# Performance work log

Hardware: AMD Instinct MI355X
Metric: run time of the kernel (lower is better)

The kernel has to match this reference:

```python
import jax, jax.numpy as jnp
import numpy as np

N_HEAD = 12

def setup_inputs() -> dict:
    key = jax.random.key(0)
    k1, k2, k3 = jax.random.split(key, 3)
    B, T, C = 8, 1024, 768
    x = jax.random.normal(k1, (B, T, C), dtype=jnp.float32)
    # torch nn.Linear weight layout: [out_features, in_features]
    W_attn = jax.random.normal(k2, (3 * C, C), dtype=jnp.float32) * 0.02
    b_attn = jax.random.normal(k3, (3 * C,), dtype=jnp.float32) * 0.02
    return {"x": x, "W_attn": W_attn, "b_attn": b_attn}

def reference(x, W_attn, b_attn):
    B, T, C = x.shape
    H = N_HEAD
    hs = C // H
    scale = 1.0 / jnp.sqrt(jnp.asarray(hs, x.dtype))
    # fused qkv projection: x @ W^T + b  -> [B, T, 3C]
    qkv = jnp.einsum('btc,oc->bto', x, W_attn) + b_attn
    qkv = qkv.reshape(B, T, 3, H, hs).transpose(2, 0, 3, 1, 4)  # [3, B, H, T, hs]
    q, k, v = qkv[0], qkv[1], qkv[2]
    scores = jnp.einsum('bhqd,bhkd->bhqk', q, k) * scale  # [B, H, T, T]
    causal = jnp.tril(jnp.ones((T, T), dtype=bool))
    # masked_fill(-inf) followed by ReLU == zero out masked positions after ReLU
    att = jnp.where(causal, jax.nn.relu(scores), jnp.zeros((), scores.dtype))
    y = jnp.einsum('bhqk,bhkd->bhqd', att, v)  # [B, H, T, hs]
    return y.transpose(0, 2, 1, 3).reshape(B, T, C)
```

## Files before the change

kernel.cpp:

```cpp
#include <hip/hip_runtime.h>
#include <hip/hip_bf16.h>
#include <stdint.h>

#define T_ 1024
#define C_ 768
#define H_ 12
#define HS 64

typedef __attribute__((ext_vector_type(8))) short bf16x8;
typedef __attribute__((ext_vector_type(4))) float f32x4;

#define GLOAD16(g, l) __builtin_amdgcn_global_load_lds( \
    (const __attribute__((address_space(1))) uint32_t*)(g), \
    (__attribute__((address_space(3))) uint32_t*)(l), 16, 0, 0)

#define WAITCNT_VM(n) asm volatile("s_waitcnt vmcnt(" #n ")" ::: "memory")

__device__ __forceinline__ ushort f2b(float f) {
  uint32_t u = __builtin_bit_cast(uint32_t, f);
  u = (u + 0x7fffu + ((u >> 16) & 1u)) >> 16;
  return (ushort)u;
}

__global__ __launch_bounds__(256) void cvt_bf16(
    const float* __restrict__ x, const float* __restrict__ wt,
    ushort* __restrict__ xb, ushort* __restrict__ wb) {
  const int NX4 = 8192 * 768 / 4;
  const int NW4 = 2304 * 768 / 4;
  int i = blockIdx.x * 256 + threadIdx.x;
  int stride = gridDim.x * 256;
  for (int idx = i; idx < NX4; idx += stride) {
    float4 f = ((const float4*)x)[idx];
    ushort4 o;
    o.x = f2b(f.x); o.y = f2b(f.y); o.z = f2b(f.z); o.w = f2b(f.w);
    ((ushort4*)xb)[idx] = o;
  }
  for (int idx = i; idx < NW4; idx += stride) {
    float4 f = ((const float4*)wt)[idx];
    ushort4 o;
    o.x = f2b(f.x); o.y = f2b(f.y); o.z = f2b(f.z); o.w = f2b(f.w);
    ((ushort4*)wb)[idx] = o;
  }
}

__global__ __launch_bounds__(256) void qkv_gemm(
    const ushort* __restrict__ xb, const ushort* __restrict__ wb,
    const float* __restrict__ bias,
    ushort* __restrict__ qo, ushort* __restrict__ ko, ushort* __restrict__ vT) {
  __shared__ __align__(16) char smem[49152];
  const int tid = threadIdx.x, lane = tid & 63, w = tid >> 6;
  const int g = lane >> 4, l15 = lane & 15;
  const int id = blockIdx.x;
  const int wg = (id & 7) * 144 + (id >> 3);
  const int m0 = (wg / 18) * 128, n0 = (wg % 18) * 128;
  const int wr = w >> 1, wc = w & 1;
  f32x4 acc[4][4] = {};

  const ushort* srcA[2];
  const ushort* srcB[2];
  int dstoff[2];
  #pragma unroll
  for (int c = 0; c < 2; ++c) {
    int p = (c * 4 + w) * 64 + lane;
    int row = p >> 2, s = p & 3;
    int sc = (s ^ ((row >> 1) & 3)) * 8;
    srcA[c] = xb + (size_t)(m0 + row) * 768 + sc;
    srcB[c] = wb + (size_t)(n0 + row) * 768 + sc;
    dstoff[c] = (c * 4 + w) * 1024;
  }

#define STAGE_G(bb_, k0) do { \
    _Pragma("unroll") \
    for (int c_ = 0; c_ < 2; ++c_) { \
      GLOAD16(srcA[c_] + (k0), (bb_) + dstoff[c_]); \
      GLOAD16(srcB[c_] + (k0), (bb_) + 8192 + dstoff[c_]); \
    } \
  } while (0)

#define GEMM_COMPUTE(cb_) do { \
    bf16x8 af[4], bfr[4]; \
    _Pragma("unroll") \
    for (int mi = 0; mi < 4; ++mi) { \
      int r_ = wr * 64 + mi * 16 + l15; \
      af[mi] = *(const bf16x8*)((cb_) + r_ * 64 + ((g ^ ((r_ >> 1) & 3)) << 4)); \
    } \
    _Pragma("unroll") \
    for (int ni = 0; ni < 4; ++ni) { \
      int r_ = wc * 64 + ni * 16 + l15; \
      bfr[ni] = *(const bf16x8*)((cb_) + 8192 + r_ * 64 + ((g ^ ((r_ >> 1) & 3)) << 4)); \
    } \
    __builtin_amdgcn_s_setprio(1); \
    _Pragma("unroll") \
    for (int mi = 0; mi < 4; ++mi) \
      _Pragma("unroll") \
      for (int ni = 0; ni < 4; ++ni) \
        acc[mi][ni] = __builtin_amdgcn_mfma_f32_16x16x32_bf16(af[mi], bfr[ni], acc[mi][ni], 0, 0, 0); \
    __builtin_amdgcn_s_setprio(0); \
  } while (0)

  STAGE_G(smem, 0);
  STAGE_G(smem + 16384, 32);
  char* cptr = smem;
  char* sptr = smem + 32768;
  for (int kk = 0; kk < 23; ++kk) {
    WAITCNT_VM(4);
    __builtin_amdgcn_s_barrier();
    if (kk < 22) STAGE_G(sptr, (kk + 2) * 32);
    GEMM_COMPUTE(cptr);
    cptr += 16384; if (cptr == smem + 49152) cptr = smem;
    sptr += 16384; if (sptr == smem + 49152) sptr = smem;
  }
  WAITCNT_VM(0);
  __builtin_amdgcn_s_barrier();
  GEMM_COMPUTE(cptr);
  __syncthreads();

  const int which = n0 / 768;
  if (which < 2) {
    ushort* outp = (which == 0) ? qo : ko;
    #pragma unroll
    for (int ni = 0; ni < 4; ++ni) {
      float bn = bias[n0 + wc * 64 + ni * 16 + l15];
      int nl = wc * 64 + ni * 16 + l15;
      #pragma unroll
      for (int mi = 0; mi < 4; ++mi) {
        #pragma unroll
        for (int r = 0; r < 4; ++r) {
          int ml = wr * 64 + mi * 16 + g * 4 + r;
          *(ushort*)(smem + ml * 256 + ((nl * 2) ^ ((ml & 7) << 4))) =
              f2b(acc[mi][ni][r] + bn);
        }
      }
    }
    __syncthreads();
    #pragma unroll
    for (int c = 0; c < 8; ++c) {
      int p = c * 256 + tid;
      int ml = p >> 4, nch = p & 15;
      uint4 val = *(const uint4*)(smem + ml * 256 + ((nch * 16) ^ ((ml & 7) << 4)));
      int m = m0 + ml;
      int nin = n0 + nch * 8 - which * 768;
      int h = nin >> 6, d = nin & 63;
      *(uint4*)(outp + ((size_t)((m >> 10) * H_ + h) * T_ + (m & (T_ - 1))) * HS + d) = val;
    }
  } else {
    #pragma unroll
    for (int ni = 0; ni < 4; ++ni) {
      float bn = bias[n0 + wc * 64 + ni * 16 + l15];
      int dl = wc * 64 + ni * 16 + l15;
      #pragma unroll
      for (int mi = 0; mi < 4; ++mi) {
        #pragma unroll
        for (int r = 0; r < 4; ++r) {
          int tl = wr * 64 + mi * 16 + g * 4 + r;
          *(ushort*)(smem + dl * 256 + ((tl * 2) ^ ((dl & 7) << 4))) =
              f2b(acc[mi][ni][r] + bn);
        }
      }
    }
    __syncthreads();
    const int b = m0 >> 10, t0base = m0 & 1023;
    #pragma unroll
    for (int c = 0; c < 8; ++c) {
      int p = c * 256 + tid;
      int dl = p >> 4, tch = p & 15;
      uint4 val = *(const uint4*)(smem + dl * 256 + ((tch * 16) ^ ((dl & 7) << 4)));
      int nin = n0 + dl - 1536;
      int h = nin >> 6, dd = nin & 63;
      *(uint4*)(vT + (((size_t)(b * H_ + h) * HS + dd) << 10) + t0base + tch * 8) = val;
    }
  }
}

__global__ __launch_bounds__(256) void attn_relu(
    const ushort* __restrict__ q, const ushort* __restrict__ k,
    const ushort* __restrict__ vT, float* __restrict__ out) {
  __shared__ __align__(16) char smem[57344];
  const int tid = threadIdx.x, lane = tid & 63, w = tid >> 6;
  const int g = lane >> 4, l15 = lane & 15;
  const int id = blockIdx.x;
  const int wg = (id & 7) * 192 + (id >> 3);
  const int bh = wg >> 4;
  const int qt = 15 - (wg & 15);
  const int q0 = qt * 64;
  const size_t base = (size_t)bh * (T_ * HS);
  const int qrow = w * 16 + l15;

  bf16x8 qf[2];
  #pragma unroll
  for (int kd = 0; kd < 2; ++kd)
    qf[kd] = *(const bf16x8*)(q + base + (size_t)(q0 + qrow) * HS + (kd * 4 + g) * 8);

  int rowS[2], scS[2], dstoff[2];
  #pragma unroll
  for (int c = 0; c < 2; ++c) {
    int p = (c * 4 + w) * 64 + lane;
    rowS[c] = p >> 3;
    scS[c] = ((p & 7) ^ (rowS[c] & 7)) * 8;
    dstoff[c] = (c * 4 + w) * 1024;
  }

#define STAGE_KV(bb_, kt) do { \
    _Pragma("unroll") \
    for (int c_ = 0; c_ < 2; ++c_) { \
      GLOAD16(k + base + (size_t)((kt) * 64 + rowS[c_]) * HS + scS[c_], (bb_) + dstoff[c_]); \
      GLOAD16(vT + base + (size_t)rowS[c_] * T_ + (kt) * 64 + scS[c_], (bb_) + 8192 + dstoff[c_]); \
    } \
  } while (0)

  f32x4 yacc[4] = {};
  char* const Pb = smem + 49152;

#define ATTN_COMPUTE(cb_, kt) do { \
    const char* Kb = (cb_); \
    const char* Vb = (cb_) + 8192; \
    f32x4 sacc[4] = {}; \
    __builtin_amdgcn_s_setprio(1); \
    _Pragma("unroll") \
    for (int kd = 0; kd < 2; ++kd) { \
      _Pragma("unroll") \
      for (int nt = 0; nt < 4; ++nt) { \
        int kr = nt * 16 + l15; \
        bf16x8 kf = *(const bf16x8*)(Kb + kr * 128 + (((kd * 4 + g) ^ (kr & 7)) << 4)); \
        sacc[nt] = __builtin_amdgcn_mfma_f32_16x16x32_bf16(qf[kd], kf, sacc[nt], 0, 0, 0); \
      } \
    } \
    __builtin_amdgcn_s_setprio(0); \
    _Pragma("unroll") \
    for (int nt = 0; nt < 4; ++nt) { \
      int kj = (kt) * 64 + nt * 16 + l15; \
      _Pragma("unroll") \
      for (int r = 0; r < 4; ++r) { \
        int i_ = w * 16 + g * 4 + r; \
        float sv = sacc[nt][r] * 0.125f; \
        float pv = (kj <= q0 + i_) ? fmaxf(sv, 0.0f) : 0.0f; \
        *(ushort*)(Pb + i_ * 128 + (((nt * 16 + l15) * 2) ^ ((i_ & 7) << 4))) = f2b(pv); \
      } \
    } \
    bf16x8 pf[2], vf[2][4]; \
    _Pragma("unroll") \
    for (int kj2 = 0; kj2 < 2; ++kj2) { \
      pf[kj2] = *(const bf16x8*)(Pb + qrow * 128 + (((kj2 * 4 + g) ^ (qrow & 7)) << 4)); \
      _Pragma("unroll") \
      for (int nt = 0; nt < 4; ++nt) { \
        int vr = nt * 16 + l15; \
        vf[kj2][nt] = *(const bf16x8*)(Vb + vr * 128 + (((kj2 * 4 + g) ^ (vr & 7)) << 4)); \
      } \
    } \
    __builtin_amdgcn_s_setprio(1); \
    _Pragma("unroll") \
    for (int kj2 = 0; kj2 < 2; ++kj2) \
      _Pragma("unroll") \
      for (int nt = 0; nt < 4; ++nt) \
        yacc[nt] = __builtin_amdgcn_mfma_f32_16x16x32_bf16(pf[kj2], vf[kj2][nt], yacc[nt], 0, 0, 0); \
    __builtin_amdgcn_s_setprio(0); \
  } while (0)

  const int nkt = qt + 1;
  STAGE_KV(smem, 0);
  if (nkt > 1) STAGE_KV(smem + 16384, 1);
  char* cptr = smem;
  char* sptr = smem + 32768;
  for (int kt = 0; kt < nkt - 1; ++kt) {
    WAITCNT_VM(4);
    __builtin_amdgcn_s_barrier();
    if (kt + 2 < nkt) STAGE_KV(sptr, kt + 2);
    ATTN_COMPUTE(cptr, kt);
    cptr += 16384; if (cptr == smem + 49152) cptr = smem;
    sptr += 16384; if (sptr == smem + 49152) sptr = smem;
  }
  WAITCNT_VM(0);
  __builtin_amdgcn_s_barrier();
  ATTN_COMPUTE(cptr, nkt - 1);

  const int bb = bh / H_, hh = bh % H_;
  #pragma unroll
  for (int nt = 0; nt < 4; ++nt) {
    #pragma unroll
    for (int r = 0; r < 4; ++r) {
      int t = q0 + w * 16 + g * 4 + r;
      int col = hh * HS + nt * 16 + l15;
      out[(size_t)(bb * T_ + t) * C_ + col] = yacc[nt][r];
    }
  }
}

extern "C" void kernel_launch(void* const* d_in, const int* in_sizes, int n_in,
                              void* d_out, int out_size, void* d_ws, size_t ws_size,
                              hipStream_t stream) {
  const float* x    = (const float*)d_in[0];
  const float* W    = (const float*)d_in[1];
  const float* bias = (const float*)d_in[2];
  float* out = (float*)d_out;

  char* ws = (char*)d_ws;
  ushort* xb = (ushort*)ws;
  ushort* wb = (ushort*)(ws + 12582912);
  ushort* qb = (ushort*)(ws + 16121856);
  ushort* kb = (ushort*)(ws + 28704768);
  ushort* vT = (ushort*)(ws + 41287680);

  cvt_bf16<<<2048, 256, 0, stream>>>(x, W, xb, wb);
  qkv_gemm<<<1152, 256, 0, stream>>>(xb, wb, bias, qb, kb, vT);
  attn_relu<<<1536, 256, 0, stream>>>(qb, kb, vT, out);
}
```

Baseline: 166.7 us.

## Rework causal ReLU attention to 32x32 MFMA with register P, deepen GEMM pipeline

```diff
diff --git a/kernel.cpp b/kernel.cpp
--- a/kernel.cpp
+++ b/kernel.cpp
@@ -9,6 +9,7 @@
 
 typedef __attribute__((ext_vector_type(8))) short bf16x8;
 typedef __attribute__((ext_vector_type(4))) float f32x4;
+typedef __attribute__((ext_vector_type(16))) float f32x16;
 
 #define GLOAD16(g, l) __builtin_amdgcn_global_load_lds( \
     (const __attribute__((address_space(1))) uint32_t*)(g), \
@@ -20,6 +21,12 @@
   uint32_t u = __builtin_bit_cast(uint32_t, f);
   u = (u + 0x7fffu + ((u >> 16) & 1u)) >> 16;
   return (ushort)u;
+}
+
+__device__ __forceinline__ uint cvtpk(float a, float b) {
+  uint r;
+  asm("v_cvt_pk_bf16_f32 %0, %1, %2" : "=v"(r) : "v"(a), "v"(b));
+  return r;
 }
 
 __global__ __launch_bounds__(256) void cvt_bf16(
@@ -47,7 +54,7 @@
     const ushort* __restrict__ xb, const ushort* __restrict__ wb,
     const float* __restrict__ bias,
     ushort* __restrict__ qo, ushort* __restrict__ ko, ushort* __restrict__ vT) {
-  __shared__ __align__(16) char smem[49152];
+  __shared__ __align__(16) char smem[81920];
   const int tid = threadIdx.x, lane = tid & 63, w = tid >> 6;
   const int g = lane >> 4, l15 = lane & 15;
   const int id = blockIdx.x;
@@ -100,15 +107,19 @@
 
   STAGE_G(smem, 0);
   STAGE_G(smem + 16384, 32);
+  STAGE_G(smem + 32768, 64);
+  STAGE_G(smem + 49152, 96);
   char* cptr = smem;
-  char* sptr = smem + 32768;
+  char* sptr = smem + 65536;
   for (int kk = 0; kk < 23; ++kk) {
-    WAITCNT_VM(4);
+    if (kk <= 20)      WAITCNT_VM(12);
+    else if (kk == 21) WAITCNT_VM(8);
+    else               WAITCNT_VM(4);
     __builtin_amdgcn_s_barrier();
-    if (kk < 22) STAGE_G(sptr, (kk + 2) * 32);
+    if (kk < 20) STAGE_G(sptr, (kk + 4) * 32);
     GEMM_COMPUTE(cptr);
-    cptr += 16384; if (cptr == smem + 49152) cptr = smem;
-    sptr += 16384; if (sptr == smem + 49152) sptr = smem;
+    cptr += 16384; if (cptr == smem + 81920) cptr = smem;
+    sptr += 16384; if (sptr == smem + 81920) sptr = smem;
   }
   WAITCNT_VM(0);
   __builtin_amdgcn_s_barrier();
@@ -172,116 +183,109 @@
   }
 }
 
-__global__ __launch_bounds__(256) void attn_relu(
+__global__ __launch_bounds__(512, 4) void attn_relu(
     const ushort* __restrict__ q, const ushort* __restrict__ k,
     const ushort* __restrict__ vT, float* __restrict__ out) {
-  __shared__ __align__(16) char smem[57344];
+  __shared__ __align__(16) char smem[49152];
   const int tid = threadIdx.x, lane = tid & 63, w = tid >> 6;
-  const int g = lane >> 4, l15 = lane & 15;
-  const int id = blockIdx.x;
-  const int wg = (id & 7) * 192 + (id >> 3);
-  const int bh = wg >> 4;
-  const int qt = 15 - (wg & 15);
-  const int q0 = qt * 64;
+  const int l31 = lane & 31, h = lane >> 5;
+  const int raw = blockIdx.x;
+  const int chunk = 3 - (raw / 96);
+  const int bh = raw % 96;
   const size_t base = (size_t)bh * (T_ * HS);
-  const int qrow = w * 16 + l15;
-
-  bf16x8 qf[2];
+  const int q0w = chunk * 256 + w * 32;
+  const int nkt = chunk * 4 + 4;
+
+  bf16x8 qf[4];
   #pragma unroll
-  for (int kd = 0; kd < 2; ++kd)
-    qf[kd] = *(const bf16x8*)(q + base + (size_t)(q0 + qrow) * HS + (kd * 4 + g) * 8);
-
-  int rowS[2], scS[2], dstoff[2];
-  #pragma unroll
-  for (int c = 0; c < 2; ++c) {
-    int p = (c * 4 + w) * 64 + lane;
-    rowS[c] = p >> 3;
-    scS[c] = ((p & 7) ^ (rowS[c] & 7)) * 8;
-    dstoff[c] = (c * 4 + w) * 1024;
-  }
+  for (int s = 0; s < 4; ++s)
+    qf[s] = *(const bf16x8*)(q + base + (size_t)(q0w + l31) * HS + s * 16 + h * 8);
+
+  const int rowS = tid >> 3;
+  const int colS = ((tid & 7) ^ (rowS & 7)) * 8;
+  const int dstS = tid * 16;
 
 #define STAGE_KV(bb_, kt) do { \
-    _Pragma("unroll") \
-    for (int c_ = 0; c_ < 2; ++c_) { \
-      GLOAD16(k + base + (size_t)((kt) * 64 + rowS[c_]) * HS + scS[c_], (bb_) + dstoff[c_]); \
-      GLOAD16(vT + base + (size_t)rowS[c_] * T_ + (kt) * 64 + scS[c_], (bb_) + 8192 + dstoff[c_]); \
+    GLOAD16(k  + base + (size_t)((kt) * 64 + rowS) * HS + colS, (bb_) + dstS); \
+    GLOAD16(vT + base + (size_t)rowS * T_ + (kt) * 64 + colS, (bb_) + 8192 + dstS); \
+  } while (0)
+
+  f32x16 yacc0 = {}, yacc1 = {};
+
+#define ATTN_TILE(cb_, kt) do { \
+    const char* Kb = (cb_); \
+    const char* Vb = (cb_) + 8192; \
+    _Pragma("unroll") \
+    for (int kr = 0; kr < 2; ++kr) { \
+      int kbase = (kt) * 64 + kr * 32; \
+      if (kbase <= q0w + 31) { \
+        f32x16 sacc = {}; \
+        int arow = kr * 32 + l31; \
+        __builtin_amdgcn_s_setprio(1); \
+        _Pragma("unroll") \
+        for (int s = 0; s < 4; ++s) { \
+          bf16x8 kf = *(const bf16x8*)(Kb + arow * 128 + (((2 * s + h) ^ (arow & 7)) << 4)); \
+          sacc = __builtin_amdgcn_mfma_f32_32x32x16_bf16(kf, qf[s], sacc, 0, 0, 0); \
+        } \
+        __builtin_amdgcn_s_setprio(0); \
+        const bool fullk = (kbase + 31 <= q0w); \
+        uint wds[8]; \
+        _Pragma("unroll") \
+        for (int i = 0; i < 8; ++i) { \
+          float a = fmaxf(sacc[2 * i] * 0.125f, 0.0f); \
+          float b = fmaxf(sacc[2 * i + 1] * 0.125f, 0.0f); \
+          if (!fullk) { \
+            int r0 = 2 * i, r1 = 2 * i + 1; \
+            if (kbase + (r0 & 3) + 8 * (r0 >> 2) + 4 * h > q0w + l31) a = 0.0f; \
+            if (kbase + (r1 & 3) + 8 * (r1 >> 2) + 4 * h > q0w + l31) b = 0.0f; \
+          } \
+          wds[i] = cvtpk(a, b); \
+        } \
+        __builtin_amdgcn_s_setprio(1); \
+        _Pragma("unroll") \
+        for (int t = 0; t < 2; ++t) { \
+          int4 pw = { (int)wds[4 * t], (int)wds[4 * t + 1], \
+                      (int)wds[4 * t + 2], (int)wds[4 * t + 3] }; \
+          bf16x8 pa = __builtin_bit_cast(bf16x8, pw); \
+          _Pragma("unroll") \
+          for (int dt = 0; dt < 2; ++dt) { \
+            int d = dt * 32 + l31; \
+            uint2 lo = *(const uint2*)(Vb + d * 128 + (((4 * kr + 2 * t) ^ (d & 7)) << 4) + 8 * h); \
+            uint2 hi = *(const uint2*)(Vb + d * 128 + (((4 * kr + 2 * t + 1) ^ (d & 7)) << 4) + 8 * h); \
+            int4 vv = { (int)lo.x, (int)lo.y, (int)hi.x, (int)hi.y }; \
+            bf16x8 vf = __builtin_bit_cast(bf16x8, vv); \
+            if (dt == 0) yacc0 = __builtin_amdgcn_mfma_f32_32x32x16_bf16(pa, vf, yacc0, 0, 0, 0); \
+            else         yacc1 = __builtin_amdgcn_mfma_f32_32x32x16_bf16(pa, vf, yacc1, 0, 0, 0); \
+          } \
+        } \
+        __builtin_amdgcn_s_setprio(0); \
+      } \
     } \
   } while (0)
 
-  f32x4 yacc[4] = {};
-  char* const Pb = smem + 49152;
-
-#define ATTN_COMPUTE(cb_, kt) do { \
-    const char* Kb = (cb_); \
-    const char* Vb = (cb_) + 8192; \
-    f32x4 sacc[4] = {}; \
-    __builtin_amdgcn_s_setprio(1); \
-    _Pragma("unroll") \
-    for (int kd = 0; kd < 2; ++kd) { \
-      _Pragma("unroll") \
-      for (int nt = 0; nt < 4; ++nt) { \
-        int kr = nt * 16 + l15; \
-        bf16x8 kf = *(const bf16x8*)(Kb + kr * 128 + (((kd * 4 + g) ^ (kr & 7)) << 4)); \
-        sacc[nt] = __builtin_amdgcn_mfma_f32_16x16x32_bf16(qf[kd], kf, sacc[nt], 0, 0, 0); \
-      } \
-    } \
-    __builtin_amdgcn_s_setprio(0); \
-    _Pragma("unroll") \
-    for (int nt = 0; nt < 4; ++nt) { \
-      int kj = (kt) * 64 + nt * 16 + l15; \
-      _Pragma("unroll") \
-      for (int r = 0; r < 4; ++r) { \
-        int i_ = w * 16 + g * 4 + r; \
-        float sv = sacc[nt][r] * 0.125f; \
-        float pv = (kj <= q0 + i_) ? fmaxf(sv, 0.0f) : 0.0f; \
-        *(ushort*)(Pb + i_ * 128 + (((nt * 16 + l15) * 2) ^ ((i_ & 7) << 4))) = f2b(pv); \
-      } \
-    } \
-    bf16x8 pf[2], vf[2][4]; \
-    _Pragma("unroll") \
-    for (int kj2 = 0; kj2 < 2; ++kj2) { \
-      pf[kj2] = *(const bf16x8*)(Pb + qrow * 128 + (((kj2 * 4 + g) ^ (qrow & 7)) << 4)); \
-      _Pragma("unroll") \
-      for (int nt = 0; nt < 4; ++nt) { \
-        int vr = nt * 16 + l15; \
-        vf[kj2][nt] = *(const bf16x8*)(Vb + vr * 128 + (((kj2 * 4 + g) ^ (vr & 7)) << 4)); \
-      } \
-    } \
-    __builtin_amdgcn_s_setprio(1); \
-    _Pragma("unroll") \
-    for (int kj2 = 0; kj2 < 2; ++kj2) \
-      _Pragma("unroll") \
-      for (int nt = 0; nt < 4; ++nt) \
-        yacc[nt] = __builtin_amdgcn_mfma_f32_16x16x32_bf16(pf[kj2], vf[kj2][nt], yacc[nt], 0, 0, 0); \
-    __builtin_amdgcn_s_setprio(0); \
-  } while (0)
-
-  const int nkt = qt + 1;
   STAGE_KV(smem, 0);
   if (nkt > 1) STAGE_KV(smem + 16384, 1);
   char* cptr = smem;
   char* sptr = smem + 32768;
   for (int kt = 0; kt < nkt - 1; ++kt) {
-    WAITCNT_VM(4);
+    WAITCNT_VM(2);
     __builtin_amdgcn_s_barrier();
     if (kt + 2 < nkt) STAGE_KV(sptr, kt + 2);
-    ATTN_COMPUTE(cptr, kt);
+    ATTN_TILE(cptr, kt);
     cptr += 16384; if (cptr == smem + 49152) cptr = smem;
     sptr += 16384; if (sptr == smem + 49152) sptr = smem;
   }
   WAITCNT_VM(0);
   __builtin_amdgcn_s_barrier();
-  ATTN_COMPUTE(cptr, nkt - 1);
+  ATTN_TILE(cptr, nkt - 1);
 
   const int bb = bh / H_, hh = bh % H_;
   #pragma unroll
-  for (int nt = 0; nt < 4; ++nt) {
-    #pragma unroll
-    for (int r = 0; r < 4; ++r) {
-      int t = q0 + w * 16 + g * 4 + r;
-      int col = hh * HS + nt * 16 + l15;
-      out[(size_t)(bb * T_ + t) * C_ + col] = yacc[nt][r];
-    }
+  for (int r = 0; r < 16; ++r) {
+    int qrow = q0w + (r & 3) + 8 * (r >> 2) + 4 * h;
+    float* op = out + (size_t)(bb * T_ + qrow) * C_ + hh * HS;
+    op[l31] = yacc0[r];
+    op[32 + l31] = yacc1[r];
   }
 }
 
@@ -302,5 +306,5 @@
 
   cvt_bf16<<<2048, 256, 0, stream>>>(x, W, xb, wb);
   qkv_gemm<<<1152, 256, 0, stream>>>(xb, wb, bias, qb, kb, vT);
-  attn_relu<<<1536, 256, 0, stream>>>(qb, kb, vT, out);
-}
+  attn_relu<<<384, 512, 0, stream>>>(qb, kb, vT, out);
+}
```

Result: faster. 153.5 us (-7.9%).
